# Kernel optimization log

Hardware: AMD Instinct MI355X
Metric: run time of the kernel (lower is better)

Reference implementation:

```python
import jax, jax.numpy as jnp
import numpy as np

# SLAYER SRM-alpha neuron / simulation constants (from network.yaml defaults)
THETA = 10.0      # spike threshold
TAU_SR = 10.0     # synaptic response time constant
TAU_REF = 2.0     # refractory time constant
SCALE_REF = 2.0   # refractory scale (kernel amplitude = -SCALE_REF*THETA)
TAU_RHO = 1.0     # surrogate-gradient width
SCALE_RHO = 1.0   # surrogate-gradient scale
TS = 1.0          # simulation step
K_PSP = 100       # truncation length of srm (alpha) kernel, ~10*tauSr
K_REF = 32        # truncation length of refractory kernel


def srm_kernel():
    t = jnp.arange(K_PSP, dtype=jnp.float32) * TS
    return (t / TAU_SR) * jnp.exp(1.0 - t / TAU_SR)  # eps(t), eps(0)=0


def ref_kernel():
    t = jnp.arange(K_REF, dtype=jnp.float32) * TS
    return -SCALE_REF * THETA * (t / TAU_REF) * jnp.exp(1.0 - t / TAU_REF)  # nu(t), nu(0)=0


def psp(z):
    # causal temporal convolution with srm kernel: u[t] = sum_k eps[k] * z[t-k]
    B, F, T = z.shape
    k = srm_kernel()[::-1].reshape(1, 1, K_PSP).astype(z.dtype)
    x = z.reshape(B * F, 1, T)
    y = jax.lax.conv_general_dilated(
        x, k, window_strides=(1,), padding=[(K_PSP - 1, 0)],
        dimension_numbers=('NCH', 'OIH', 'NCH'))
    return y.reshape(B, F, T)


@jax.custom_vjp
def spike_fn(u):
    return (u >= THETA).astype(u.dtype)

def _spike_fwd(u):
    return spike_fn(u), u

def _spike_bwd(u, g):
    # SLAYER surrogate spike pdf: scaleRho/(tauRho*theta) * exp(-|u-theta|/(tauRho*theta))
    pdf = (SCALE_RHO / (TAU_RHO * THETA)) * jnp.exp(-jnp.abs(u - THETA) / (TAU_RHO * THETA))
    return (g * pdf,)

spike_fn.defvjp(_spike_fwd, _spike_bwd)


def spike_dyn(u):
    # sequential LIF threshold with refractory response added to future potentials
    B, F, T = u.shape
    ref = ref_kernel().astype(u.dtype)  # [K_REF]

    def step(buf, u_t):  # buf: [B,F,K_REF] pending refractory contributions
        v = u_t + buf[..., 0]
        s = spike_fn(v)
        buf = buf + s[..., None] * ref
        buf = jnp.concatenate([buf[..., 1:], jnp.zeros_like(buf[..., :1])], axis=-1)
        return buf, s

    buf0 = jnp.zeros((B, F, K_REF), u.dtype)
    _, spikes = jax.lax.scan(step, buf0, jnp.moveaxis(u, 2, 0))  # [T,B,F]
    return jnp.moveaxis(spikes, 0, 2)


def slayer_layer(x, W):
    # dense (per-timestep GEMM, no bias) -> psp -> spike
    z = jnp.einsum('bft,of->bot', x, W)
    return spike_dyn(psp(z))


def setup_inputs() -> dict:
    key = jax.random.key(0)
    k0, k1, k2, k3 = jax.random.split(key, 4)
    B, F_IN, T = 8, 128 * 128, 300
    inp = (jax.random.uniform(k0, (B, F_IN, T)) < 0.1).astype(jnp.float32)
    W1 = jax.random.normal(k1, (410, F_IN), jnp.float32) * 0.05
    W2 = jax.random.normal(k2, (240, 410), jnp.float32) * 0.3
    W3 = jax.random.normal(k3, (10, 240), jnp.float32) * 0.3
    return {"input": inp, "W1": W1, "W2": W2, "W3": W3}


def reference(input, W1, W2, W3):
    x = slayer_layer(input, W1)
    x = slayer_layer(x, W2)
    x = slayer_layer(x, W3)
    return x  # [B, 10, T] spike trains
```

## Files before the change

kernel.cpp:

```cpp
#include <hip/hip_runtime.h>


#define B   8
#define T   300
#define F0  16384
#define O1  410
#define O2  240
#define OP2 240
#define O3  10
#define OP3 16
#define W1M 7
#define W2M 4
#define NCOLS (B*T)
#define LCAP 2048
#define PPLC32 ((size_t)416 * NCOLS)

typedef int  int32x4  __attribute__((ext_vector_type(4)));
typedef int  int32x16 __attribute__((ext_vector_type(16)));

__device__ __forceinline__ int32x4 expand16(unsigned m)
{
    int32x4 r;
    r.x = (int)((((m      ) & 15u) * 0x00204081u) & 0x01010101u);
    r.y = (int)((((m >>  4) & 15u) * 0x00204081u) & 0x01010101u);
    r.z = (int)((((m >>  8) & 15u) * 0x00204081u) & 0x01010101u);
    r.w = (int)((((m >> 12) & 15u) * 0x00204081u) & 0x01010101u);
    return r;
}

__global__ __launch_bounds__(256) void prep_kernel(
    const float* __restrict__ X,  const float* __restrict__ W1,
    const float* __restrict__ W2, const float* __restrict__ W3,
    unsigned short* __restrict__ Bbit, char* __restrict__ Aswz,
    int* __restrict__ Q2T, int* __restrict__ Q3T)
{
    __shared__ float tileT[64][65];
    int bid = blockIdx.x;
    int tid = threadIdx.x;

    if (bid < 10240) {
        int tt = bid % 5, fb = (bid / 5) % 256, b = bid / 1280;
        int t0 = tt * 64, f0 = fb * 64;
        const float* Xb = X + ((size_t)b * F0 + f0) * T;
        int fl = tid >> 4;
        int tq = (tid & 15) * 4;
        #pragma unroll
        for (int i = 0; i < 4; ++i) {
            int fr = fl + i * 16;
            int t  = t0 + tq;
            float4 v = make_float4(0.f, 0.f, 0.f, 0.f);
            if (t < T) v = *(const float4*)(Xb + (size_t)fr * T + t);
            tileT[tq + 0][fr] = v.x;
            tileT[tq + 1][fr] = v.y;
            tileT[tq + 2][fr] = v.z;
            tileT[tq + 3][fr] = v.w;
        }
        __syncthreads();
        int sub = tid & 3;
        int tl  = tid >> 2;
        unsigned m = 0u;
        #pragma unroll
        for (int j = 0; j < 16; ++j)
            m |= (tileT[tl][sub * 16 + j] != 0.0f ? 1u : 0u) << j;
        int t = t0 + tl;
        if (t < T)
            Bbit[((size_t)(b * 256 + fb) * 320 + t) * 4 + sub] = (unsigned short)m;

    } else if (bid < 11904) {
        int j = bid - 10240;
        int o  = j >> 2;
        int f0 = ((j & 3) * 256 + tid) * 16;

        float w[16];
        if (o < O1) {
            #pragma unroll
            for (int e = 0; e < 16; e += 4)
                *(float4*)&w[e] = *(const float4*)(W1 + (size_t)o * F0 + f0 + e);
        } else {
            #pragma unroll
            for (int e = 0; e < 16; ++e) w[e] = 0.0f;
        }

        unsigned pk[4][4] = {{0,0,0,0},{0,0,0,0},{0,0,0,0},{0,0,0,0}};
        #pragma unroll
        for (int e = 0; e < 16; ++e) {
            int q = (int)__double2ll_rn((double)w[e] * 134217728.0);
            int l0 = (int)(signed char)(q & 255);  q = (q - l0) >> 8;
            int l1 = (int)(signed char)(q & 255);  q = (q - l1) >> 8;
            int l2 = (int)(signed char)(q & 255);  int l3 = (q - l2) >> 8;
            pk[0][e >> 2] |= (unsigned)(l0 & 255) << (8 * (e & 3));
            pk[1][e >> 2] |= (unsigned)(l1 & 255) << (8 * (e & 3));
            pk[2][e >> 2] |= (unsigned)(l2 & 255) << (8 * (e & 3));
            pk[3][e >> 2] |= (unsigned)(l3 & 255) << (8 * (e & 3));
        }

        int kit = f0 >> 6, ks = (f0 >> 5) & 1, hb = (f0 >> 4) & 1;
        #pragma unroll
        for (int l = 0; l < 4; ++l) {
            int m = o * 4 + l;
            int mt = m >> 7, r = m & 127, g = r >> 5, row = r & 31;
            int word = ks * 64 + row + 32 * hb;
            size_t addr = ((size_t)(mt * 256 + kit) * 4 + g) * 2048 + (size_t)word * 16;
            *(int32x4*)(Aswz + addr) =
                (int32x4){(int)pk[l][0], (int)pk[l][1], (int)pk[l][2], (int)pk[l][3]};
        }

    } else {
        int idx = (bid - 11904) * 256 + tid;
        const int n1 = O1 * OP2;
        const int n2 = O2 * OP3;
        if (idx < n1) {
            int f = idx / OP2, o = idx - f * OP2;
            Q2T[idx] = (int)__double2ll_rn((double)W2[(size_t)o * O1 + f] * 67108864.0);
        } else if (idx < n1 + n2) {
            int j = idx - n1;
            int f = j / OP3, o = j - f * OP3;
            double v = (o < O3) ? (double)W3[(size_t)o * O2 + f] : 0.0;
            Q3T[j] = (int)__double2ll_rn(v * 67108864.0);
        }
    }
}

__global__ __launch_bounds__(256) void mfma_gemm_kernel(
    const char* __restrict__ Aswz, const unsigned short* __restrict__ Bbit,
    int* __restrict__ Pc)
{
    int id  = blockIdx.x;
    int xcd = id & 7, rr = id >> 3;
    int bh  = rr & 15, gq = rr >> 4;
    int g   = xcd + 8 * gq;
    int mt = g >> 3, kc = g & 7;
    int b = bh >> 1, half = bh & 1;

    int tid = threadIdx.x;
    int lane = tid & 63, wv = tid >> 6;
    int wm = wv >> 1, wn = wv & 1;
    int ng0 = wn * 3;
    int nfr = wn ? 2 : 3;

    const char* Ab = Aswz + ((size_t)(mt * 256 + kc * 32) * 4 + wm * 2) * 2048
                          + (size_t)lane * 16;
    const char* Bb = (const char*)Bbit + (size_t)(b * 256 + kc * 32) * 320 * 8;
    int hb16 = (lane >> 5) * 16;

    const char* Bf[3];
    #pragma unroll
    for (int fn = 0; fn < 3; ++fn) {
        int colf = (half * 5 + ng0 + fn) * 32 + (lane & 31);
        Bf[fn] = Bb + (size_t)colf * 8;
    }

    int32x16 acc[2][3];
    #pragma unroll
    for (int fm = 0; fm < 2; ++fm)
        #pragma unroll
        for (int fn = 0; fn < 3; ++fn)
            acc[fm][fn] = (int32x16){0,0,0,0,0,0,0,0,0,0,0,0,0,0,0,0};

    int32x4 aA[2][2], aB[2][2];
    uint2   rA[3],    rB[3];

#define LOAD_STAGE(AR, RR, ITN)                                               \
    { const char* Abn_ = Ab + (size_t)(ITN) * 8192;                           \
      AR[0][0] = *(const int32x4*)(Abn_);                                     \
      AR[0][1] = *(const int32x4*)(Abn_ + 1024);                              \
      AR[1][0] = *(const int32x4*)(Abn_ + 2048);                              \
      AR[1][1] = *(const int32x4*)(Abn_ + 3072);                              \
      _Pragma("unroll")                                                       \
      for (int fn_ = 0; fn_ < 3; ++fn_)                                       \
          if (fn_ < nfr)                                                      \
              RR[fn_] = *(const uint2*)(Bf[fn_] + (size_t)(ITN) * 2560); }

#define COMPUTE_STAGE(AR, RR)                                                 \
    { _Pragma("unroll")                                                       \
      for (int ks_ = 0; ks_ < 2; ++ks_)                                       \
          _Pragma("unroll")                                                   \
          for (int fn_ = 0; fn_ < 3; ++fn_)                                   \
              if (fn_ < nfr) {                                                \
                  unsigned mraw_ = ks_ ? RR[fn_].y : RR[fn_].x;               \
                  int32x4 bvv_ = expand16((mraw_ >> hb16) & 0xFFFFu);         \
                  acc[0][fn_] = __builtin_amdgcn_mfma_i32_32x32x32_i8(        \
                      AR[0][ks_], bvv_, acc[0][fn_], 0, 0, 0);                \
                  acc[1][fn_] = __builtin_amdgcn_mfma_i32_32x32x32_i8(        \
                      AR[1][ks_], bvv_, acc[1][fn_], 0, 0, 0);                \
              } }

    LOAD_STAGE(aA, rA, 0);
    for (int it = 0; it < 32; it += 2) {
        LOAD_STAGE(aB, rB, it + 1);
        COMPUTE_STAGE(aA, rA);
        int itn2 = (it + 2 < 32) ? it + 2 : 31;
        LOAD_STAGE(aA, rA, itn2);
        COMPUTE_STAGE(aB, rB);
    }
#undef LOAD_STAGE
#undef COMPUTE_STAGE

    int col = lane & 31, h = lane >> 5;
    int* Pk = Pc + (size_t)kc * PPLC32 + (size_t)b * T;
    #pragma unroll
    for (int fm = 0; fm < 2; ++fm) {
        #pragma unroll
        for (int fn = 0; fn < 3; ++fn) {
            if (fn >= nfr) continue;
            int t = (half * 5 + ng0 + fn) * 32 + col;
            if (t >= T) continue;
            int obase = mt * 32 + wm * 16 + fm * 8;
            #pragma unroll
            for (int q = 0; q < 4; ++q) {
                int o = obase + 2 * q + h;
                unsigned s = (unsigned)acc[fm][fn][4 * q]
                           + ((unsigned)acc[fm][fn][4 * q + 1] << 8)
                           + ((unsigned)acc[fm][fn][4 * q + 2] << 16)
                           + ((unsigned)acc[fm][fn][4 * q + 3] << 24);
                Pk[(size_t)o * NCOLS + t] = (int)s;
            }
        }
    }
}

__global__ __launch_bounds__(320) void redpsp1_kernel(
    const int* __restrict__ Pc, unsigned short* __restrict__ smask)
{
    __shared__ double zs[16][304];
    __shared__ double us[16][304];
    __shared__ double eps[100];
    int og = blockIdx.x, b = blockIdx.y;
    int o0 = og * 16;
    int tid = threadIdx.x;
    const double sc27 = 1.0 / 134217728.0;

    if (tid < 100) {
        double td = (double)tid;
        eps[tid] = (td / 10.0) * exp(1.0 - td / 10.0);
    }
    if (tid < T) {
        size_t col = (size_t)b * T + tid;
        #pragma unroll 4
        for (int ol = 0; ol < 16; ++ol) {
            int o = o0 + ol;
            size_t idx = (size_t)o * NCOLS + col;
            long long s = 0;
            #pragma unroll
            for (int c = 0; c < 8; ++c)
                s += (long long)Pc[(size_t)c * PPLC32 + idx];
            zs[ol][tid] = (double)s * sc27;
        }
    }
    __syncthreads();

    if (tid < T) {
        double sum[16];
        #pragma unroll
        for (int o = 0; o < 16; ++o) sum[o] = 0.0;
        int kmax = tid < 99 ? tid : 99;
        for (int k = 0; k <= kmax; ++k) {
            double e = eps[k];
            #pragma unroll
            for (int o = 0; o < 16; ++o)
                sum[o] = fma(e, zs[o][tid - k], sum[o]);
        }
        #pragma unroll
        for (int o = 0; o < 16; ++o) us[o][tid] = sum[o];
    }
    if (og == 25 && tid < T) {
        size_t col = (size_t)b * T + tid;
        *(unsigned*)((char*)smask + (col * 28 + 26) * 2) = 0u;
    }
    __syncthreads();

    if (tid < 64) {
        int l = tid;
        bool act = (l < 16) && (o0 + l < O1);
        const double alpha = exp(-0.5);
        const double A31   = exp(-15.5);
        const double c0    = -10.0 * exp(1.0);
        double E = 0.0, G = 0.0;
        unsigned hist = 0u;
        for (int t = 0; t < T; ++t) {
            double uval = act ? us[l][t] : -1.0e300;
            double v = uval + c0 * G;
            bool sp = (v >= 10.0);
            unsigned long long bal = __ballot(sp);
            if (l == 0)
                smask[((size_t)b * T + t) * 28 + og] =
                    (unsigned short)(bal & 0xFFFFu);
            double sN  = sp ? 1.0 : 0.0;
            double s31 = ((hist >> 30) & 1u) ? 1.0 : 0.0;
            double Em  = E - A31 * s31;
            double Gm  = G - 31.0 * A31 * s31;
            G = alpha * (sN + Gm + Em);
            E = alpha * (sN + Em);
            hist = (hist << 1) | (sp ? 1u : 0u);
        }
    }
}

template<int OPAD_, int O_, int SLOTS, int NOG, bool OUT>
__global__ __launch_bounds__(320) void redpsp23_kernel(
    const int* __restrict__ Z, unsigned short* __restrict__ smask,
    float* __restrict__ sout, double scale)
{
    __shared__ double zs[16][304];
    __shared__ double us[16][304];
    __shared__ double eps[100];
    int og = blockIdx.x, b = blockIdx.y;
    int o0 = og * 16;
    int tid = threadIdx.x;

    if (tid < 100) {
        double td = (double)tid;
        eps[tid] = (td / 10.0) * exp(1.0 - td / 10.0);
    }
    if (tid < T) {
        size_t col = (size_t)b * T + tid;
        #pragma unroll 4
        for (int ol = 0; ol < 16; ++ol) {
            int o = o0 + ol;
            double zv = (o < OPAD_) ? (double)Z[col * OPAD_ + o] * scale : 0.0;
            zs[ol][tid] = zv;
        }
    }
    __syncthreads();

    if (tid < T) {
        double sum[16];
        #pragma unroll
        for (int o = 0; o < 16; ++o) sum[o] = 0.0;
        int kmax = tid < 99 ? tid : 99;
        for (int k = 0; k <= kmax; ++k) {
            double e = eps[k];
            #pragma unroll
            for (int o = 0; o < 16; ++o)
                sum[o] = fma(e, zs[o][tid - k], sum[o]);
        }
        #pragma unroll
        for (int o = 0; o < 16; ++o) us[o][tid] = sum[o];
    }
    if (SLOTS > NOG && og == NOG - 1 && tid < T) {
        size_t col = (size_t)b * T + tid;
        #pragma unroll
        for (int s = NOG; s < SLOTS; ++s)
            smask[col * SLOTS + s] = 0;
    }
    __syncthreads();

    if (tid < 64) {
        int l = tid;
        bool act = (l < 16) && (o0 + l < O_);
        const double alpha = exp(-0.5);
        const double A31   = exp(-15.5);
        const double c0    = -10.0 * exp(1.0);
        double E = 0.0, G = 0.0;
        unsigned hist = 0u;
        for (int t = 0; t < T; ++t) {
            double uval = act ? us[l][t] : -1.0e300;
            double v = uval + c0 * G;
            bool sp = (v >= 10.0);
            unsigned long long bal = __ballot(sp);
            if (SLOTS > 0 && l == 0)
                smask[((size_t)b * T + t) * SLOTS + og] =
                    (unsigned short)(bal & 0xFFFFu);
            if (OUT && act)
                sout[((size_t)b * O_ + o0 + l) * T + t] = sp ? 1.0f : 0.0f;
            double sN  = sp ? 1.0 : 0.0;
            double s31 = ((hist >> 30) & 1u) ? 1.0 : 0.0;
            double Em  = E - A31 * s31;
            double Gm  = G - 31.0 * A31 * s31;
            G = alpha * (sN + Gm + Em);
            E = alpha * (sN + Em);
            hist = (hist << 1) | (sp ? 1u : 0u);
        }
    }
}

__global__ __launch_bounds__(128) void sparse_gemm_kernel(
    const int* __restrict__ QT, const unsigned long long* __restrict__ cmask,
    int* __restrict__ Z, int OPAD, int W, int CW, int cshift)
{
    __shared__ int lf[LCAP];
    __shared__ int wsum[2];

    int chunk = blockIdx.x & ((1 << cshift) - 1);
    int col   = blockIdx.x >> cshift;
    int tid   = threadIdx.x;

    int wbase = col * W + chunk * CW;
    unsigned long long w0 = (2 * tid     < CW) ? cmask[wbase + 2 * tid]     : 0ULL;
    unsigned long long w1 = (2 * tid + 1 < CW) ? cmask[wbase + 2 * tid + 1] : 0ULL;
    int my = __popcll(w0) + __popcll(w1);

    int scan = my;
    #pragma unroll
    for (int d = 1; d < 64; d <<= 1) {
        int v = __shfl_up(scan, d);
        if ((tid & 63) >= d) scan += v;
    }
    if ((tid & 63) == 63) wsum[tid >> 6] = scan;
    __syncthreads();
    int off = ((tid >= 64) ? wsum[0] : 0) + scan - my;
    int n = wsum[0] + wsum[1];

    int f0e = (chunk * CW + 2 * tid) * 64;
    unsigned long long m = w0;
    while (m) {
        int bit = __ffsll(m) - 1;
        if (off < LCAP) lf[off] = (f0e + bit) * OPAD;
        ++off; m &= m - 1;
    }
    m = w1; f0e += 64;
    while (m) {
        int bit = __ffsll(m) - 1;
        if (off < LCAP) lf[off] = (f0e + bit) * OPAD;
        ++off; m &= m - 1;
    }
    __syncthreads();
    if (n > LCAP) n = LCAP;

    if (tid * 4 < OPAD) {
        int o = tid * 4;
        const int* bq = QT + o;
        int a0 = 0, a1 = 0, a2 = 0, a3 = 0;
        int i = 0;
        for (; i + 8 <= n; i += 8) {
            int4 ia = *(const int4*)&lf[i];
            int4 ib = *(const int4*)&lf[i + 4];
            int e0 = __builtin_amdgcn_readfirstlane(ia.x);
            int e1 = __builtin_amdgcn_readfirstlane(ia.y);
            int e2 = __builtin_amdgcn_readfirstlane(ia.z);
            int e3 = __builtin_amdgcn_readfirstlane(ia.w);
            int e4 = __builtin_amdgcn_readfirstlane(ib.x);
            int e5 = __builtin_amdgcn_readfirstlane(ib.y);
            int e6 = __builtin_amdgcn_readfirstlane(ib.z);
            int e7 = __builtin_amdgcn_readfirstlane(ib.w);
            int4 q0 = *(const int4*)(bq + e0);
            int4 q1 = *(const int4*)(bq + e1);
            int4 q2 = *(const int4*)(bq + e2);
            int4 q3 = *(const int4*)(bq + e3);
            int4 q4 = *(const int4*)(bq + e4);
            int4 q5 = *(const int4*)(bq + e5);
            int4 q6 = *(const int4*)(bq + e6);
            int4 q7 = *(const int4*)(bq + e7);
            a0 += q0.x; a1 += q0.y; a2 += q0.z; a3 += q0.w;
            a0 += q1.x; a1 += q1.y; a2 += q1.z; a3 += q1.w;
            a0 += q2.x; a1 += q2.y; a2 += q2.z; a3 += q2.w;
            a0 += q3.x; a1 += q3.y; a2 += q3.z; a3 += q3.w;
            a0 += q4.x; a1 += q4.y; a2 += q4.z; a3 += q4.w;
            a0 += q5.x; a1 += q5.y; a2 += q5.z; a3 += q5.w;
            a0 += q6.x; a1 += q6.y; a2 += q6.z; a3 += q6.w;
            a0 += q7.x; a1 += q7.y; a2 += q7.z; a3 += q7.w;
        }
        for (; i < n; ++i) {
            int e = __builtin_amdgcn_readfirstlane(lf[i]);
            int4 q = *(const int4*)(bq + e);
            a0 += q.x; a1 += q.y; a2 += q.z; a3 += q.w;
        }
        int* zb = Z + ((size_t)chunk * NCOLS + col) * OPAD + o;
        *(int4*)zb = make_int4(a0, a1, a2, a3);
    }
}

extern "C" void kernel_launch(void* const* d_in, const int* in_sizes, int n_in,
                              void* d_out, int out_size, void* d_ws, size_t ws_size,
                              hipStream_t stream)
{
    const float* x  = (const float*)d_in[0];
    const float* W1 = (const float*)d_in[1];
    const float* W2 = (const float*)d_in[2];
    const float* W3 = (const float*)d_in[3];
    float* out = (float*)d_out;

    const size_t sz_Aswz   = (size_t)13 * 256 * 4 * 2048;
    const size_t sz_Bbit   = (size_t)B * 256 * 320 * 4 * 2;
    const size_t sz_Pc     = (size_t)8 * PPLC32 * 4;
    const size_t sz_Q2T    = (size_t)O1 * OP2 * 4;
    const size_t sz_Q3T    = (size_t)O2 * OP3 * 4;
    const size_t sz_smask1 = (size_t)NCOLS * 28 * 2;
    const size_t sz_smask2 = (size_t)NCOLS * 16 * 2;

    char* p = (char*)d_ws;
    char*           Aswz   = p;                  p += sz_Aswz;
    unsigned short* Bbit   = (unsigned short*)p; p += sz_Bbit;
    int*            Pc     = (int*)p;  char* pa = p;  p += sz_Pc;
    int*            Q2T    = (int*)p;            p += sz_Q2T;
    int*            Q3T    = (int*)p;            p += sz_Q3T;
    unsigned short* smask1 = (unsigned short*)p; p += sz_smask1;
    unsigned short* smask2 = (unsigned short*)p; p += sz_smask2;
    int* z2 = (int*)pa;                          pa += (size_t)NCOLS * OP2 * 4;
    int* z3 = (int*)pa;                          pa += (size_t)NCOLS * OP3 * 4;

    const double sc26 = 1.0 / 67108864.0;

    prep_kernel<<<dim3(12304), dim3(256), 0, stream>>>(
        x, W1, W2, W3, Bbit, Aswz, Q2T, Q3T);

    mfma_gemm_kernel<<<dim3(1664), dim3(256), 0, stream>>>(Aswz, Bbit, Pc);
    redpsp1_kernel<<<dim3(26, B), dim3(320), 0, stream>>>(Pc, smask1);

    sparse_gemm_kernel<<<dim3(NCOLS), dim3(128), 0, stream>>>(
        Q2T, (const unsigned long long*)smask1, z2, OP2, W1M, W1M, 0);
    redpsp23_kernel<OP2, O2, 16, 15, false><<<dim3(15, B), dim3(320), 0, stream>>>(
        z2, smask2, (float*)0, sc26);

    sparse_gemm_kernel<<<dim3(NCOLS), dim3(128), 0, stream>>>(
        Q3T, (const unsigned long long*)smask2, z3, OP3, W2M, W2M, 0);
    redpsp23_kernel<OP3, O3, 0, 1, true><<<dim3(1, B), dim3(320), 0, stream>>>(
        z3, (unsigned short*)0, out, sc26);
}
```

Baseline: 259.9 us.

## Fuse sparse spike GEMM into PSP/spike kernels for layers two and three

Removes the standalone sparse_gemm kernels for layers 2 and 3. Each thread of the PSP kernel now walks its column's input spike bitmask and accumulates the 16 quantized weight rows for its output group directly into registers, writing them to shared memory. This drops two kernel launches and the global Z round-trip. In exchange each of the 15 output-group blocks re-scans the same bitmask, and per-thread divergent bit loops run over only 120 blocks instead of 2400, which lowers parallelism.

```diff
diff --git a/kernel.cpp b/kernel.cpp
--- a/kernel.cpp
+++ b/kernel.cpp
@@ -9,10 +9,7 @@
 #define OP2 240
 #define O3  10
 #define OP3 16
-#define W1M 7
-#define W2M 4
 #define NCOLS (B*T)
-#define LCAP 2048
 #define PPLC32 ((size_t)416 * NCOLS)
 
 typedef int  int32x4  __attribute__((ext_vector_type(4)));
@@ -296,10 +293,10 @@
     }
 }
 
-template<int OPAD_, int O_, int SLOTS, int NOG, bool OUT>
-__global__ __launch_bounds__(320) void redpsp23_kernel(
-    const int* __restrict__ Z, unsigned short* __restrict__ smask,
-    float* __restrict__ sout, double scale)
+template<int FINW, int OPAD_, int O_, int NOG, int SLOTS_OUT, bool OUT>
+__global__ __launch_bounds__(320) void redpsp_sp_kernel(
+    const int* __restrict__ QT, const unsigned long long* __restrict__ inmask,
+    unsigned short* __restrict__ omask, float* __restrict__ sout, double scale)
 {
     __shared__ double zs[16][304];
     __shared__ double us[16][304];
@@ -314,12 +311,35 @@
     }
     if (tid < T) {
         size_t col = (size_t)b * T + tid;
-        #pragma unroll 4
-        for (int ol = 0; ol < 16; ++ol) {
-            int o = o0 + ol;
-            double zv = (o < OPAD_) ? (double)Z[col * OPAD_ + o] * scale : 0.0;
-            zs[ol][tid] = zv;
-        }
+        unsigned long long mw[FINW];
+        #pragma unroll
+        for (int w = 0; w < FINW; ++w)
+            mw[w] = inmask[col * FINW + w];
+
+        int ac[16];
+        #pragma unroll
+        for (int i = 0; i < 16; ++i) ac[i] = 0;
+
+        #pragma unroll
+        for (int w = 0; w < FINW; ++w) {
+            unsigned long long m = mw[w];
+            while (m) {
+                int f = w * 64 + __ffsll(m) - 1;
+                m &= m - 1;
+                const int* qp = QT + (size_t)f * OPAD_ + o0;
+                int4 q0 = *(const int4*)(qp);
+                int4 q1 = *(const int4*)(qp + 4);
+                int4 q2 = *(const int4*)(qp + 8);
+                int4 q3 = *(const int4*)(qp + 12);
+                ac[0]  += q0.x; ac[1]  += q0.y; ac[2]  += q0.z; ac[3]  += q0.w;
+                ac[4]  += q1.x; ac[5]  += q1.y; ac[6]  += q1.z; ac[7]  += q1.w;
+                ac[8]  += q2.x; ac[9]  += q2.y; ac[10] += q2.z; ac[11] += q2.w;
+                ac[12] += q3.x; ac[13] += q3.y; ac[14] += q3.z; ac[15] += q3.w;
+            }
+        }
+        #pragma unroll
+        for (int ol = 0; ol < 16; ++ol)
+            zs[ol][tid] = (double)ac[ol] * scale;
     }
     __syncthreads();
 
@@ -337,11 +357,11 @@
         #pragma unroll
         for (int o = 0; o < 16; ++o) us[o][tid] = sum[o];
     }
-    if (SLOTS > NOG && og == NOG - 1 && tid < T) {
+    if (SLOTS_OUT > NOG && og == NOG - 1 && tid < T) {
         size_t col = (size_t)b * T + tid;
         #pragma unroll
-        for (int s = NOG; s < SLOTS; ++s)
-            smask[col * SLOTS + s] = 0;
+        for (int s = NOG; s < SLOTS_OUT; ++s)
+            omask[col * SLOTS_OUT + s] = 0;
     }
     __syncthreads();
 
@@ -358,8 +378,8 @@
             double v = uval + c0 * G;
             bool sp = (v >= 10.0);
             unsigned long long bal = __ballot(sp);
-            if (SLOTS > 0 && l == 0)
-                smask[((size_t)b * T + t) * SLOTS + og] =
+            if (SLOTS_OUT > 0 && l == 0)
+                omask[((size_t)b * T + t) * SLOTS_OUT + og] =
                     (unsigned short)(bal & 0xFFFFu);
             if (OUT && act)
                 sout[((size_t)b * O_ + o0 + l) * T + t] = sp ? 1.0f : 0.0f;
@@ -374,92 +394,6 @@
     }
 }
 
-__global__ __launch_bounds__(128) void sparse_gemm_kernel(
-    const int* __restrict__ QT, const unsigned long long* __restrict__ cmask,
-    int* __restrict__ Z, int OPAD, int W, int CW, int cshift)
-{
-    __shared__ int lf[LCAP];
-    __shared__ int wsum[2];
-
-    int chunk = blockIdx.x & ((1 << cshift) - 1);
-    int col   = blockIdx.x >> cshift;
-    int tid   = threadIdx.x;
-
-    int wbase = col * W + chunk * CW;
-    unsigned long long w0 = (2 * tid     < CW) ? cmask[wbase + 2 * tid]     : 0ULL;
-    unsigned long long w1 = (2 * tid + 1 < CW) ? cmask[wbase + 2 * tid + 1] : 0ULL;
-    int my = __popcll(w0) + __popcll(w1);
-
-    int scan = my;
-    #pragma unroll
-    for (int d = 1; d < 64; d <<= 1) {
-        int v = __shfl_up(scan, d);
-        if ((tid & 63) >= d) scan += v;
-    }
-    if ((tid & 63) == 63) wsum[tid >> 6] = scan;
-    __syncthreads();
-    int off = ((tid >= 64) ? wsum[0] : 0) + scan - my;
-    int n = wsum[0] + wsum[1];
-
-    int f0e = (chunk * CW + 2 * tid) * 64;
-    unsigned long long m = w0;
-    while (m) {
-        int bit = __ffsll(m) - 1;
-        if (off < LCAP) lf[off] = (f0e + bit) * OPAD;
-        ++off; m &= m - 1;
-    }
-    m = w1; f0e += 64;
-    while (m) {
-        int bit = __ffsll(m) - 1;
-        if (off < LCAP) lf[off] = (f0e + bit) * OPAD;
-        ++off; m &= m - 1;
-    }
-    __syncthreads();
-    if (n > LCAP) n = LCAP;
-
-    if (tid * 4 < OPAD) {
-        int o = tid * 4;
-        const int* bq = QT + o;
-        int a0 = 0, a1 = 0, a2 = 0, a3 = 0;
-        int i = 0;
-        for (; i + 8 <= n; i += 8) {
-            int4 ia = *(const int4*)&lf[i];
-            int4 ib = *(const int4*)&lf[i + 4];
-            int e0 = __builtin_amdgcn_readfirstlane(ia.x);
-            int e1 = __builtin_amdgcn_readfirstlane(ia.y);
-            int e2 = __builtin_amdgcn_readfirstlane(ia.z);
-            int e3 = __builtin_amdgcn_readfirstlane(ia.w);
-            int e4 = __builtin_amdgcn_readfirstlane(ib.x);
-            int e5 = __builtin_amdgcn_readfirstlane(ib.y);
-            int e6 = __builtin_amdgcn_readfirstlane(ib.z);
-            int e7 = __builtin_amdgcn_readfirstlane(ib.w);
-            int4 q0 = *(const int4*)(bq + e0);
-            int4 q1 = *(const int4*)(bq + e1);
-            int4 q2 = *(const int4*)(bq + e2);
-            int4 q3 = *(const int4*)(bq + e3);
-            int4 q4 = *(const int4*)(bq + e4);
-            int4 q5 = *(const int4*)(bq + e5);
-            int4 q6 = *(const int4*)(bq + e6);
-            int4 q7 = *(const int4*)(bq + e7);
-            a0 += q0.x; a1 += q0.y; a2 += q0.z; a3 += q0.w;
-            a0 += q1.x; a1 += q1.y; a2 += q1.z; a3 += q1.w;
-            a0 += q2.x; a1 += q2.y; a2 += q2.z; a3 += q2.w;
-            a0 += q3.x; a1 += q3.y; a2 += q3.z; a3 += q3.w;
-            a0 += q4.x; a1 += q4.y; a2 += q4.z; a3 += q4.w;
-            a0 += q5.x; a1 += q5.y; a2 += q5.z; a3 += q5.w;
-            a0 += q6.x; a1 += q6.y; a2 += q6.z; a3 += q6.w;
-            a0 += q7.x; a1 += q7.y; a2 += q7.z; a3 += q7.w;
-        }
-        for (; i < n; ++i) {
-            int e = __builtin_amdgcn_readfirstlane(lf[i]);
-            int4 q = *(const int4*)(bq + e);
-            a0 += q.x; a1 += q.y; a2 += q.z; a3 += q.w;
-        }
-        int* zb = Z + ((size_t)chunk * NCOLS + col) * OPAD + o;
-        *(int4*)zb = make_int4(a0, a1, a2, a3);
-    }
-}
-
 extern "C" void kernel_launch(void* const* d_in, const int* in_sizes, int n_in,
                               void* d_out, int out_size, void* d_ws, size_t ws_size,
                               hipStream_t stream)
@@ -481,13 +415,11 @@
     char* p = (char*)d_ws;
     char*           Aswz   = p;                  p += sz_Aswz;
     unsigned short* Bbit   = (unsigned short*)p; p += sz_Bbit;
-    int*            Pc     = (int*)p;  char* pa = p;  p += sz_Pc;
+    int*            Pc     = (int*)p;            p += sz_Pc;
     int*            Q2T    = (int*)p;            p += sz_Q2T;
     int*            Q3T    = (int*)p;            p += sz_Q3T;
     unsigned short* smask1 = (unsigned short*)p; p += sz_smask1;
     unsigned short* smask2 = (unsigned short*)p; p += sz_smask2;
-    int* z2 = (int*)pa;                          pa += (size_t)NCOLS * OP2 * 4;
-    int* z3 = (int*)pa;                          pa += (size_t)NCOLS * OP3 * 4;
 
     const double sc26 = 1.0 / 67108864.0;
 
@@ -497,13 +429,9 @@
     mfma_gemm_kernel<<<dim3(1664), dim3(256), 0, stream>>>(Aswz, Bbit, Pc);
     redpsp1_kernel<<<dim3(26, B), dim3(320), 0, stream>>>(Pc, smask1);
 
-    sparse_gemm_kernel<<<dim3(NCOLS), dim3(128), 0, stream>>>(
-        Q2T, (const unsigned long long*)smask1, z2, OP2, W1M, W1M, 0);
-    redpsp23_kernel<OP2, O2, 16, 15, false><<<dim3(15, B), dim3(320), 0, stream>>>(
-        z2, smask2, (float*)0, sc26);
-
-    sparse_gemm_kernel<<<dim3(NCOLS), dim3(128), 0, stream>>>(
-        Q3T, (const unsigned long long*)smask2, z3, OP3, W2M, W2M, 0);
-    redpsp23_kernel<OP3, O3, 0, 1, true><<<dim3(1, B), dim3(320), 0, stream>>>(
-        z3, (unsigned short*)0, out, sc26);
-}
+    redpsp_sp_kernel<7, OP2, O2, 15, 16, false><<<dim3(15, B), dim3(320), 0, stream>>>(
+        Q2T, (const unsigned long long*)smask1, smask2, (float*)0, sc26);
+
+    redpsp_sp_kernel<4, OP3, O3, 1, 0, true><<<dim3(1, B), dim3(320), 0, stream>>>(
+        Q3T, (const unsigned long long*)smask2, (unsigned short*)0, out, sc26);
+}
```

Result: slower. 278.1 us (+7.0%).
